# Kernel tuning notes

Measured on AMD Instinct MI355X. Metric: run time of the kernel, lower is better.

## Reference

```python
import jax, jax.numpy as jnp
import numpy as np

# Model constants (match init_kwargs)
IN_DIM = 1024   # input_dim == OLA frame size
ST_DIM = 128    # state_dim
HOP = IN_DIM // 2
N_FRAMES = 512
N_SAMPLES = 262144  # n_frames * hop
CTX = 512       # context_dim == control_plane_dim
HD = 32         # hypernetwork_dim
HL = 16         # hypernetwork_latent
B = 8


def _make_w(hv, A, Bm, i, o):
    # HyperNetworkLayer: hypervector -> latent -> flattened (i, o) matrix per batch
    return (hv @ A @ Bm).reshape(-1, i, o)


def setup_inputs() -> dict:
    key = jax.random.key(0)
    ks = jax.random.split(key, 17)
    s = 0.05
    return {
        'control_signal': jax.random.normal(ks[0], (B, CTX, N_FRAMES), jnp.float32),
        'state_hv': jax.random.normal(ks[1], (B, HD), jnp.float32),
        'output_hv': jax.random.normal(ks[2], (B, HD), jnp.float32),
        'input_hv': jax.random.normal(ks[3], (B, HD), jnp.float32),
        'direct_hv': jax.random.normal(ks[4], (B, HD), jnp.float32),
        'proj_hv': jax.random.normal(ks[5], (B, HD), jnp.float32),
        'times': jax.random.normal(ks[6], (B, 1, N_FRAMES), jnp.float32),
        # hypernetwork parameters (learned)
        'A_proj': jax.random.normal(ks[7], (HD, HL), jnp.float32) * s,
        'B_proj': jax.random.normal(ks[8], (HL, CTX * IN_DIM), jnp.float32) * s,
        'A_state': jax.random.normal(ks[9], (HD, HL), jnp.float32) * s,
        'B_state': jax.random.normal(ks[10], (HL, ST_DIM * ST_DIM), jnp.float32) * s,
        'A_input': jax.random.normal(ks[11], (HD, HL), jnp.float32) * s,
        'B_input': jax.random.normal(ks[12], (HL, IN_DIM * ST_DIM), jnp.float32) * s,
        'A_output': jax.random.normal(ks[13], (HD, HL), jnp.float32) * s,
        'B_output': jax.random.normal(ks[14], (HL, ST_DIM * IN_DIM), jnp.float32) * s,
        'A_direct': jax.random.normal(ks[15], (HD, HL), jnp.float32) * s,
        'B_direct': jax.random.normal(ks[16], (HL, IN_DIM * IN_DIM), jnp.float32) * s,
    }


def _forward(control_signal, state_hv, output_hv, input_hv, direct_hv, proj_hv, times,
             A_proj, B_proj, A_state, B_state, A_input, B_input,
             A_output, B_output, A_direct, B_direct):
    batch = control_signal.shape[0]
    dt = control_signal.dtype
    # per-batch hypernetwork-generated dense matrices
    Wp = _make_w(proj_hv, A_proj, B_proj, CTX, IN_DIM)       # [b, ctx, in]
    Ws = _make_w(state_hv, A_state, B_state, ST_DIM, ST_DIM)  # [b, st, st]
    Wi = _make_w(input_hv, A_input, B_input, IN_DIM, ST_DIM)  # [b, in, st]
    Wo = _make_w(output_hv, A_output, B_output, ST_DIM, IN_DIM)
    Wd = _make_w(direct_hv, A_direct, B_direct, IN_DIM, IN_DIM)

    ctrl = jnp.transpose(control_signal ** 2, (0, 2, 1))       # [b, fr, ctx]
    proj = jnp.einsum('bfc,bci->bfi', ctrl, Wp)                # [b, fr, in]

    def step(s, u):
        # s_i = A s_{i-1} + B u_i ; y_i = C (A s_{i-1}) + D u_i
        s2 = jnp.einsum('bs,bst->bt', s, Ws)
        y = jnp.einsum('bt,bti->bi', s2, Wo) + jnp.einsum('bi,bij->bj', u, Wd)
        s_new = s2 + jnp.einsum('bi,bis->bs', u, Wi)
        return s_new, y

    s0 = jnp.zeros((batch, ST_DIM), dt)
    _, outs = jax.lax.scan(step, s0, jnp.transpose(proj, (1, 0, 2)))  # [fr, b, in]
    outs = jnp.transpose(outs, (1, 0, 2))                              # [b, fr, in]

    # overlap-add with periodic hann window, hop = in_dim // 2
    win = 0.5 - 0.5 * jnp.cos(2.0 * jnp.pi * jnp.arange(IN_DIM, dtype=dt) / IN_DIM)
    windowed = outs * win
    total = HOP * (N_FRAMES - 1) + IN_DIM
    idx = jnp.arange(N_FRAMES)[:, None] * HOP + jnp.arange(IN_DIM)[None, :]  # [fr, in]
    buf = jnp.zeros((batch, total), dt).at[:, idx].add(windowed)
    sig = buf[:, :N_SAMPLES][:, None, :]   # [b, 1, n_samples]

    # DiracScheduler.schedule: softmax impulses over frames, upsample, FFT convolve
    impulses = jax.nn.softmax(times, axis=-1)                  # [b, 1, fr]
    up = jnp.zeros((batch, 1, N_SAMPLES), dt).at[:, :, ::N_SAMPLES // N_FRAMES].set(impulses)
    n = 2 * N_SAMPLES
    y = jnp.fft.irfft(jnp.fft.rfft(sig, n=n) * jnp.fft.rfft(up, n=n), n=n)[..., :N_SAMPLES]
    return y.astype(dt)


def reference(control_signal, state_hv, output_hv, input_hv, direct_hv, proj_hv, times,
              A_proj, B_proj, A_state, B_state, A_input, B_input,
              A_output, B_output, A_direct, B_direct):
    return _forward(control_signal, state_hv, output_hv, input_hv, direct_hv, proj_hv, times,
                    A_proj, B_proj, A_state, B_state, A_input, B_input,
                    A_output, B_output, A_direct, B_direct)
```

## Files before the change

kernel.cpp:

```cpp
#include <hip/hip_runtime.h>
#include <math.h>


typedef __attribute__((ext_vector_type(8))) short bfrag;
typedef __attribute__((ext_vector_type(4))) float f32x4;

__device__ inline unsigned short f2bf(float f) {
  unsigned int u = __float_as_uint(f);
  unsigned int r = (u + 0x7fff + ((u >> 16) & 1)) >> 16;
  return (unsigned short)r;
}

static const size_t OFF_LAT   = 0;
static const size_t OFF_IMP   = 1024;
static const size_t OFF_WSM   = 8192;
static const size_t OFF_WPT   = 139264;
static const size_t OFF_WOT   = 2236416;
static const size_t OFF_WDIT  = 2760704;
static const size_t OFF_CTRLT = 7479296;
static const size_t OFF_PROJ  = 8527872;
static const size_t OFF_PROJD = 10625024;
static const size_t OFF_S2    = 15343616;
static const size_t OFF_MPOW  = 15605760;
static const size_t OFF_EC    = 16785408;
static const size_t OFF_HC    = 16850944;
static const size_t OFF_Y     = 16916480;
static const size_t OFF_SIG   = 21110784;
static const size_t OFF_T     = 23207936;

__global__ void latents_kernel(
    const float* __restrict__ hv_p, const float* __restrict__ hv_s,
    const float* __restrict__ hv_i, const float* __restrict__ hv_o,
    const float* __restrict__ hv_d,
    const float* __restrict__ A_p, const float* __restrict__ A_s,
    const float* __restrict__ A_i, const float* __restrict__ A_o,
    const float* __restrict__ A_d,
    float* __restrict__ lat) {
  int tid = threadIdx.x;
  if (tid >= 640) return;
  int m = tid >> 7, b = (tid >> 4) & 7, l = tid & 15;
  const float* hv; const float* A;
  switch (m) {
    case 0: hv = hv_p; A = A_p; break;
    case 1: hv = hv_s; A = A_s; break;
    case 2: hv = hv_i; A = A_i; break;
    case 3: hv = hv_o; A = A_o; break;
    default: hv = hv_d; A = A_d; break;
  }
  float acc = 0.f;
  for (int h = 0; h < 32; ++h) acc = fmaf(hv[b * 32 + h], A[h * 16 + l], acc);
  lat[tid] = acc;
}

__global__ __launch_bounds__(256) void build_w_kernel(
    const float* __restrict__ lat,
    const float* __restrict__ Bm,
    float* __restrict__ out,
    int total, size_t bstride) {
  int e = (blockIdx.x * 256 + threadIdx.x) * 4;
  if (e >= total) return;
  float4 v[16];
#pragma unroll
  for (int l = 0; l < 16; ++l)
    v[l] = *(const float4*)(Bm + (size_t)l * total + e);
#pragma unroll 1
  for (int b = 0; b < 8; ++b) {
    float ax = 0.f, ay = 0.f, az = 0.f, aw = 0.f;
#pragma unroll
    for (int l = 0; l < 16; ++l) {
      float lv = lat[b * 16 + l];
      ax = fmaf(lv, v[l].x, ax);
      ay = fmaf(lv, v[l].y, ay);
      az = fmaf(lv, v[l].z, az);
      aw = fmaf(lv, v[l].w, aw);
    }
    *(float4*)(out + (size_t)b * bstride + e) = make_float4(ax, ay, az, aw);
  }
}

__global__ __launch_bounds__(256) void build_wt_kernel(
    const float* __restrict__ lat,
    const float* __restrict__ Bm,
    unsigned short* __restrict__ out,
    int R, int C, size_t bstride) {
  __shared__ float ls[128];
  __shared__ unsigned short tile[32][36];
  int tid = threadIdx.x;
  if (tid < 128) ls[tid] = lat[tid];
  int cc = tid & 31, rg = tid >> 5;
  int c = blockIdx.x * 32 + cc;
  int r0 = blockIdx.y * 32 + rg * 4;
  size_t RC = (size_t)R * C;
  float bm[16][4];
#pragma unroll
  for (int l = 0; l < 16; ++l) {
    const float* p = Bm + (size_t)l * RC + (size_t)r0 * C + c;
#pragma unroll
    for (int j = 0; j < 4; ++j) bm[l][j] = p[(size_t)j * C];
  }
  int wc = tid >> 3, wrq = tid & 7;
  __syncthreads();
#pragma unroll 1
  for (int b = 0; b < 8; ++b) {
    float a0 = 0.f, a1 = 0.f, a2 = 0.f, a3 = 0.f;
#pragma unroll
    for (int l = 0; l < 16; ++l) {
      float lv = ls[b * 16 + l];
      a0 = fmaf(lv, bm[l][0], a0);
      a1 = fmaf(lv, bm[l][1], a1);
      a2 = fmaf(lv, bm[l][2], a2);
      a3 = fmaf(lv, bm[l][3], a3);
    }
    __syncthreads();
    ushort2 p0, p1;
    p0.x = f2bf(a0); p0.y = f2bf(a1);
    p1.x = f2bf(a2); p1.y = f2bf(a3);
    *(ushort2*)&tile[cc][rg * 4] = p0;
    *(ushort2*)&tile[cc][rg * 4 + 2] = p1;
    __syncthreads();
    ushort4 v = *(const ushort4*)&tile[wc][wrq * 4];
    *(ushort4*)(out + (size_t)b * bstride +
                (size_t)(blockIdx.x * 32 + wc) * R + blockIdx.y * 32 + wrq * 4) = v;
  }
}

__global__ void transpose_sq_kernel(const float* __restrict__ in,
                                    unsigned short* __restrict__ out) {
  __shared__ float tile[32][33];
  int b = blockIdx.z;
  int c0 = blockIdx.x * 32, f0 = blockIdx.y * 32;
  int tx = threadIdx.x, ty = threadIdx.y;
  const float* inb = in + (size_t)b * 512 * 512;
  unsigned short* outb = out + (size_t)b * 512 * 512;
#pragma unroll
  for (int i = 0; i < 4; ++i) {
    float v = inb[(size_t)(c0 + ty + i * 8) * 512 + f0 + tx];
    tile[ty + i * 8][tx] = v * v;
  }
  __syncthreads();
#pragma unroll
  for (int i = 0; i < 4; ++i)
    outb[(size_t)(f0 + ty + i * 8) * 512 + c0 + tx] = f2bf(tile[tx][ty + i * 8]);
}

template <int EPI, int CD_BF16, int TRI>
__global__ __launch_bounds__(256) void mfma_gemm_kernel(
    const unsigned short* __restrict__ A,
    const unsigned short* __restrict__ BT,
    const float* __restrict__ D, int ldd,
    void* __restrict__ Cout,
    int M, int N, int K) {
  const int b = blockIdx.z;
  A  += (size_t)b * M * K;
  BT += (size_t)b * N * K;
  const int m0 = blockIdx.y * 128;
  const int n0 = blockIdx.x * 128;
  __shared__ __align__(16) unsigned short As[128][40];
  __shared__ __align__(16) unsigned short Bs[128][40];
  const int tid = threadIdx.x;
  const int lane = tid & 63, wave = tid >> 6;
  const int wr = (wave >> 1) * 64, wc = (wave & 1) * 64;
  const int l15 = lane & 15, g = lane >> 4;
  f32x4 acc[4][4];
#pragma unroll
  for (int i = 0; i < 4; ++i)
#pragma unroll
    for (int j = 0; j < 4; ++j)
#pragma unroll
      for (int r = 0; r < 4; ++r) acc[i][j][r] = 0.f;

  const int srow = tid >> 2, soct = tid & 3;
  const unsigned short* Ag = A + (size_t)(m0 + srow) * K + soct * 8;
  const unsigned short* Bg = BT + (size_t)(n0 + srow) * K + soct * 8;
  const size_t row64 = (size_t)64 * K;
  const int kend = TRI ? (m0 + 128) : K;

  for (int k0 = 0; k0 < kend; k0 += 32) {
    bfrag av0 = *(const bfrag*)(Ag + k0);
    bfrag av1 = *(const bfrag*)(Ag + row64 + k0);
    bfrag bv0 = *(const bfrag*)(Bg + k0);
    bfrag bv1 = *(const bfrag*)(Bg + row64 + k0);
    __syncthreads();
    *(bfrag*)(&As[srow][soct * 8]) = av0;
    *(bfrag*)(&As[64 + srow][soct * 8]) = av1;
    *(bfrag*)(&Bs[srow][soct * 8]) = bv0;
    *(bfrag*)(&Bs[64 + srow][soct * 8]) = bv1;
    __syncthreads();
    bfrag af[4], bf[4];
#pragma unroll
    for (int mi = 0; mi < 4; ++mi)
      af[mi] = *(const bfrag*)(&As[wr + mi * 16 + l15][g * 8]);
#pragma unroll
    for (int nj = 0; nj < 4; ++nj)
      bf[nj] = *(const bfrag*)(&Bs[wc + nj * 16 + l15][g * 8]);
#pragma unroll
    for (int mi = 0; mi < 4; ++mi)
#pragma unroll
      for (int nj = 0; nj < 4; ++nj)
        acc[mi][nj] = __builtin_amdgcn_mfma_f32_16x16x32_bf16(af[mi], bf[nj], acc[mi][nj], 0, 0, 0);
  }

  float* Cf = (float*)Cout + (size_t)b * M * N;
  unsigned short* Cb = (unsigned short*)Cout + (size_t)b * M * N;
  if (EPI) D += (size_t)b * M * ldd;
#pragma unroll
  for (int nj = 0; nj < 4; ++nj) {
    int n = n0 + wc + nj * 16 + l15;
    float win = 0.f;
    if (EPI) win = 0.5f - 0.5f * cosf(6.28318530717958647693f * (float)n / 1024.0f);
#pragma unroll
    for (int mi = 0; mi < 4; ++mi) {
      int mbase = m0 + wr + mi * 16 + 4 * g;
#pragma unroll
      for (int r = 0; r < 4; ++r) {
        int m = mbase + r;
        float v = acc[mi][nj][r];
        if (EPI) v = (v + D[(size_t)m * ldd + n]) * win;
        if (CD_BF16) Cb[(size_t)m * N + n] = f2bf(v);
        else         Cf[(size_t)m * N + n] = v;
      }
    }
  }
}

__global__ void copym1_kernel(const float* __restrict__ Wsm, float* __restrict__ Mpow) {
  int i = blockIdx.x * 256 + threadIdx.x;
  int b = i >> 12, r = i & 4095;
  *(float4*)(Mpow + ((size_t)b * 9 + 1) * 16384 + (size_t)r * 4) =
      *(const float4*)(Wsm + (size_t)b * 16384 + (size_t)r * 4);
}

__global__ __launch_bounds__(256) void powers_kernel(float* __restrict__ Mpow, int half) {
  int z = blockIdx.x;
  int b = z / half, k = z - b * half + 1;
  const float* A = Mpow + ((size_t)b * 9 + k) * 16384;
  const float* Bm = Mpow + ((size_t)b * 9 + half) * 16384;
  float* C = Mpow + ((size_t)b * 9 + half + k) * 16384;
  __shared__ __align__(16) float As[16][132];
  __shared__ __align__(16) float Bs[16][132];
  int tid = threadIdx.x;
  int tx = tid & 15, ty = tid >> 4;
  float acc[8][8];
#pragma unroll
  for (int i = 0; i < 8; ++i)
#pragma unroll
    for (int j = 0; j < 8; ++j) acc[i][j] = 0.f;
  int ar = tid >> 1, ac = (tid & 1) * 8;
  int br = tid >> 4, bc = (tid & 15) * 8;
  for (int k0 = 0; k0 < 128; k0 += 16) {
    float4 a0 = *(const float4*)(A + (size_t)ar * 128 + k0 + ac);
    float4 a1 = *(const float4*)(A + (size_t)ar * 128 + k0 + ac + 4);
    float4 b0 = *(const float4*)(Bm + (size_t)(k0 + br) * 128 + bc);
    float4 b1 = *(const float4*)(Bm + (size_t)(k0 + br) * 128 + bc + 4);
    __syncthreads();
    As[ac + 0][ar] = a0.x; As[ac + 1][ar] = a0.y; As[ac + 2][ar] = a0.z; As[ac + 3][ar] = a0.w;
    As[ac + 4][ar] = a1.x; As[ac + 5][ar] = a1.y; As[ac + 6][ar] = a1.z; As[ac + 7][ar] = a1.w;
    *(float4*)(&Bs[br][bc]) = b0;
    *(float4*)(&Bs[br][bc + 4]) = b1;
    __syncthreads();
#pragma unroll
    for (int kk = 0; kk < 16; ++kk) {
      float4 av0 = *(const float4*)(&As[kk][ty * 8]);
      float4 av1 = *(const float4*)(&As[kk][ty * 8 + 4]);
      float4 bv0 = *(const float4*)(&Bs[kk][tx * 8]);
      float4 bv1 = *(const float4*)(&Bs[kk][tx * 8 + 4]);
      float aa[8] = {av0.x, av0.y, av0.z, av0.w, av1.x, av1.y, av1.z, av1.w};
      float bb[8] = {bv0.x, bv0.y, bv0.z, bv0.w, bv1.x, bv1.y, bv1.z, bv1.w};
#pragma unroll
      for (int i = 0; i < 8; ++i)
#pragma unroll
        for (int j = 0; j < 8; ++j) acc[i][j] = fmaf(aa[i], bb[j], acc[i][j]);
    }
  }
#pragma unroll
  for (int i = 0; i < 8; ++i) {
    *(float4*)(C + (size_t)(ty * 8 + i) * 128 + tx * 8) =
        make_float4(acc[i][0], acc[i][1], acc[i][2], acc[i][3]);
    *(float4*)(C + (size_t)(ty * 8 + i) * 128 + tx * 8 + 4) =
        make_float4(acc[i][4], acc[i][5], acc[i][6], acc[i][7]);
  }
}

__global__ __launch_bounds__(256) void ec_kernel(
    const float* __restrict__ Mpow, const float* __restrict__ PD,
    float* __restrict__ Ec) {
  int b = blockIdx.x >> 6, c = blockIdx.x & 63;
  int tid = threadIdx.x, t = tid & 127, dh = tid >> 7;
  __shared__ __align__(16) float Bus[7][128];
  __shared__ float red[128];
  const float* Bu = PD + (size_t)b * 512 * 1152 + 1024;
  for (int idx = tid; idx < 896; idx += 256)
    Bus[idx >> 7][idx & 127] = Bu[(size_t)(c * 8 + (idx >> 7)) * 1152 + (idx & 127)];
  __syncthreads();
  float acc = 0.f;
  const float* Mb = Mpow + (size_t)b * 9 * 16384;
  int d0 = dh * 64;
#pragma unroll
  for (int i = 0; i < 7; ++i) {
    const float* Mk = Mb + (size_t)(7 - i) * 16384 + t;
#pragma unroll 8
    for (int d = 0; d < 64; ++d)
      acc = fmaf(Bus[i][d0 + d], Mk[(size_t)(d0 + d) * 128], acc);
  }
  if (dh == 1) red[t] = acc;
  __syncthreads();
  if (dh == 0) {
    float tot = acc + red[t] + Bu[(size_t)(c * 8 + 7) * 1152 + t];
    Ec[((size_t)b * 64 + c) * 128 + t] = tot;
  }
}

__global__ __launch_bounds__(128) void combine_kernel(
    const float* __restrict__ Mpow, const float* __restrict__ Ec,
    float* __restrict__ Hc) {
  int b = blockIdx.x, t = threadIdx.x;
  float w[128];
  const float* M8 = Mpow + ((size_t)b * 9 + 8) * 16384;
#pragma unroll
  for (int k = 0; k < 128; ++k) w[k] = M8[(size_t)k * 128 + t];
  __shared__ __align__(16) float sh[128];
  sh[t] = 0.f;
  Hc[((size_t)b * 64) * 128 + t] = 0.f;
  __syncthreads();
#pragma unroll 1
  for (int c = 0; c < 63; ++c) {
    float a0 = 0.f, a1 = 0.f, a2 = 0.f, a3 = 0.f;
#pragma unroll
    for (int k = 0; k < 128; k += 4) {
      float4 sv = *(const float4*)(&sh[k]);
      a0 = fmaf(sv.x, w[k + 0], a0);
      a1 = fmaf(sv.y, w[k + 1], a1);
      a2 = fmaf(sv.z, w[k + 2], a2);
      a3 = fmaf(sv.w, w[k + 3], a3);
    }
    float hn = (a0 + a1) + (a2 + a3) + Ec[((size_t)b * 64 + c) * 128 + t];
    __syncthreads();
    sh[t] = hn;
    __syncthreads();
    Hc[((size_t)b * 64 + c + 1) * 128 + t] = hn;
  }
}

__global__ __launch_bounds__(256) void pass2_kernel(
    const float* __restrict__ Mpow, const float* __restrict__ PD,
    const float* __restrict__ Hc, unsigned short* __restrict__ S2) {
  int b = blockIdx.x >> 6, c = blockIdx.x & 63;
  int tid = threadIdx.x, t = tid & 127, dh = tid >> 7;
  __shared__ __align__(16) float Xs[15][128];
  __shared__ __align__(16) float red[8][128];
  const float* Bu = PD + (size_t)b * 512 * 1152 + 1024;
  for (int idx = tid; idx < 15 * 128; idx += 256) {
    int rr = idx >> 7, cc = idx & 127;
    float v = 0.f;
    if (rr == 7) v = Hc[((size_t)b * 64 + c) * 128 + cc];
    else if (rr > 7) v = Bu[(size_t)(c * 8 + rr - 8) * 1152 + cc];
    Xs[rr][cc] = v;
  }
  __syncthreads();
  float acc[8];
#pragma unroll
  for (int j = 0; j < 8; ++j) acc[j] = 0.f;
  const float* Mb = Mpow + (size_t)b * 9 * 16384;
  int d0 = dh * 64;
#pragma unroll 1
  for (int k = 1; k <= 8; ++k) {
    const float* Mk = Mb + (size_t)k * 16384 + t;
    const int xbase = 8 - k;
#pragma unroll 4
    for (int d4 = 0; d4 < 16; ++d4) {
      int d = d0 + d4 * 4;
      float m0 = Mk[(size_t)(d + 0) * 128];
      float m1 = Mk[(size_t)(d + 1) * 128];
      float m2 = Mk[(size_t)(d + 2) * 128];
      float m3 = Mk[(size_t)(d + 3) * 128];
#pragma unroll
      for (int j = 0; j < 8; ++j) {
        float4 xv = *(const float4*)(&Xs[xbase + j][d]);
        acc[j] = fmaf(xv.x, m0, acc[j]);
        acc[j] = fmaf(xv.y, m1, acc[j]);
        acc[j] = fmaf(xv.z, m2, acc[j]);
        acc[j] = fmaf(xv.w, m3, acc[j]);
      }
    }
  }
  if (dh == 1) {
#pragma unroll
    for (int j = 0; j < 8; ++j) red[j][t] = acc[j];
  }
  __syncthreads();
  if (dh == 0) {
    unsigned short* S2b = S2 + ((size_t)b * 512 + c * 8) * 128;
#pragma unroll
    for (int j = 0; j < 8; ++j)
      S2b[(size_t)j * 128 + t] = f2bf(acc[j] + red[j][t]);
  }
}

__global__ void softmax_kernel(const float* __restrict__ times, float* __restrict__ imp) {
  int b = blockIdx.x, t = threadIdx.x;
  __shared__ float red[512];
  float v = times[b * 512 + t];
  red[t] = v;
  __syncthreads();
  for (int s = 256; s > 0; s >>= 1) {
    if (t < s) red[t] = fmaxf(red[t], red[t + s]);
    __syncthreads();
  }
  float m = red[0];
  __syncthreads();
  float e = expf(v - m);
  red[t] = e;
  __syncthreads();
  for (int s = 256; s > 0; s >>= 1) {
    if (t < s) red[t] += red[t + s];
    __syncthreads();
  }
  imp[b * 512 + t] = e / red[0];
}

__global__ void toeplitz_kernel(const float* __restrict__ imp, unsigned short* __restrict__ T) {
  int idx = blockIdx.x * 256 + threadIdx.x;
  int b = idx >> 16;
  int rem = idx & 65535;
  int q = rem >> 7, p4 = (rem & 127) * 4;
  const float* impb = imp + b * 512;
  ushort4 o;
  o.x = (p4 + 0 <= q) ? f2bf(impb[q - p4 - 0]) : (unsigned short)0;
  o.y = (p4 + 1 <= q) ? f2bf(impb[q - p4 - 1]) : (unsigned short)0;
  o.z = (p4 + 2 <= q) ? f2bf(impb[q - p4 - 2]) : (unsigned short)0;
  o.w = (p4 + 3 <= q) ? f2bf(impb[q - p4 - 3]) : (unsigned short)0;
  *(ushort4*)(T + ((size_t)b * 512 + q) * 512 + p4) = o;
}

__global__ __launch_bounds__(256) void ola_t_kernel(const float* __restrict__ Y,
                                                    unsigned short* __restrict__ sigT) {
  __shared__ unsigned short tile[64][72];
  int b = blockIdx.z;
  int q0 = blockIdx.x * 64, r0 = blockIdx.y * 64;
  int tid = threadIdx.x;
  int rr = tid & 63, qg = tid >> 6;
  const float* Yb = Y + (size_t)b * 512 * 1024;
#pragma unroll
  for (int i = 0; i < 16; ++i) {
    int q = q0 + qg * 16 + i;
    float v = Yb[(size_t)q * 1024 + r0 + rr];
    if (q > 0) v += Yb[(size_t)(q - 1) * 1024 + 512 + r0 + rr];
    tile[qg * 16 + i][rr] = f2bf(v);
  }
  __syncthreads();
  int rw = tid >> 2, qo = tid & 3;
  unsigned short* outb = sigT + ((size_t)b * 512 + r0 + rw) * 512 + q0;
  *(bfrag*)(outb + qo * 16) = *(const bfrag*)&tile[qo * 16][0] ;
}


extern "C" void kernel_launch(void* const* d_in, const int* in_sizes, int n_in,
                              void* d_out, int out_size, void* d_ws, size_t ws_size,
                              hipStream_t stream);

__global__ __launch_bounds__(256) void ola_transpose_kernel(const float* __restrict__ Y,
                                                            unsigned short* __restrict__ sigT) {
  __shared__ unsigned short tile[64][72];
  int b = blockIdx.z;
  int q0 = blockIdx.x * 64, r0 = blockIdx.y * 64;
  int tid = threadIdx.x;
  int rr = tid & 63, qg = tid >> 6;
  const float* Yb = Y + (size_t)b * 512 * 1024;
#pragma unroll
  for (int i = 0; i < 16; ++i) {
    int q = q0 + qg * 16 + i;
    float v = Yb[(size_t)q * 1024 + r0 + rr];
    if (q > 0) v += Yb[(size_t)(q - 1) * 1024 + 512 + r0 + rr];
    tile[qg * 16 + i][rr] = f2bf(v);
  }
  __syncthreads();
  int rw = tid >> 2, qo = tid & 3;
  unsigned short* orow = sigT + ((size_t)b * 512 + r0 + rw) * 512 + q0 + qo * 16;
  ushort4 w0, w1, w2, w3;
  w0.x = tile[qo * 16 + 0][rw];  w0.y = tile[qo * 16 + 1][rw];
  w0.z = tile[qo * 16 + 2][rw];  w0.w = tile[qo * 16 + 3][rw];
  w1.x = tile[qo * 16 + 4][rw];  w1.y = tile[qo * 16 + 5][rw];
  w1.z = tile[qo * 16 + 6][rw];  w1.w = tile[qo * 16 + 7][rw];
  w2.x = tile[qo * 16 + 8][rw];  w2.y = tile[qo * 16 + 9][rw];
  w2.z = tile[qo * 16 + 10][rw]; w2.w = tile[qo * 16 + 11][rw];
  w3.x = tile[qo * 16 + 12][rw]; w3.y = tile[qo * 16 + 13][rw];
  w3.z = tile[qo * 16 + 14][rw]; w3.w = tile[qo * 16 + 15][rw];
  *(ushort4*)(orow + 0)  = w0;
  *(ushort4*)(orow + 4)  = w1;
  *(ushort4*)(orow + 8)  = w2;
  *(ushort4*)(orow + 12) = w3;
}

extern "C" void kernel_launch(void* const* d_in, const int* in_sizes, int n_in,
                              void* d_out, int out_size, void* d_ws, size_t ws_size,
                              hipStream_t stream) {
  const float* control   = (const float*)d_in[0];
  const float* state_hv  = (const float*)d_in[1];
  const float* output_hv = (const float*)d_in[2];
  const float* input_hv  = (const float*)d_in[3];
  const float* direct_hv = (const float*)d_in[4];
  const float* proj_hv   = (const float*)d_in[5];
  const float* times     = (const float*)d_in[6];
  const float* A_proj   = (const float*)d_in[7];
  const float* B_proj   = (const float*)d_in[8];
  const float* A_state  = (const float*)d_in[9];
  const float* B_state  = (const float*)d_in[10];
  const float* A_input  = (const float*)d_in[11];
  const float* B_input  = (const float*)d_in[12];
  const float* A_output = (const float*)d_in[13];
  const float* B_output = (const float*)d_in[14];
  const float* A_direct = (const float*)d_in[15];
  const float* B_direct = (const float*)d_in[16];

  float* ws = (float*)d_ws;
  float* lat  = ws + OFF_LAT;
  float* impw = ws + OFF_IMP;
  float* Wsm  = ws + OFF_WSM;
  unsigned short* WpT   = (unsigned short*)(ws + OFF_WPT);
  unsigned short* WoT   = (unsigned short*)(ws + OFF_WOT);
  unsigned short* WdiT  = (unsigned short*)(ws + OFF_WDIT);
  unsigned short* ctrlT = (unsigned short*)(ws + OFF_CTRLT);
  unsigned short* proj  = (unsigned short*)(ws + OFF_PROJ);
  float* projD = ws + OFF_PROJD;
  unsigned short* S2 = (unsigned short*)(ws + OFF_S2);
  float* Mpow = ws + OFF_MPOW;
  float* Ec   = ws + OFF_EC;
  float* Hc   = ws + OFF_HC;
  float* Y    = ws + OFF_Y;
  unsigned short* sigT = (unsigned short*)(ws + OFF_SIG);
  unsigned short* Tb   = (unsigned short*)(ws + OFF_T);
  float* out  = (float*)d_out;

  latents_kernel<<<1, 640, 0, stream>>>(proj_hv, state_hv, input_hv, output_hv, direct_hv,
                                        A_proj, A_state, A_input, A_output, A_direct, lat);

  build_w_kernel<<<16, 256, 0, stream>>>(lat + 1 * 128, B_state, Wsm, 16384, 16384);

  build_wt_kernel<<<dim3(32, 16), 256, 0, stream>>>(lat + 0 * 128, B_proj, WpT, 512, 1024, 524288);
  build_wt_kernel<<<dim3(32, 32), 256, 0, stream>>>(lat + 4 * 128, B_direct, WdiT, 1024, 1024, 1179648);
  build_wt_kernel<<<dim3(4, 32), 256, 0, stream>>>(lat + 2 * 128, B_input, WdiT + 1024 * 1024, 1024, 128, 1179648);
  build_wt_kernel<<<dim3(32, 4), 256, 0, stream>>>(lat + 3 * 128, B_output, WoT, 128, 1024, 131072);

  transpose_sq_kernel<<<dim3(16, 16, 8), dim3(32, 8), 0, stream>>>(control, ctrlT);

  mfma_gemm_kernel<0, 1, 0><<<dim3(8, 4, 8), 256, 0, stream>>>(
      ctrlT, WpT, nullptr, 0, proj, 512, 1024, 512);

  mfma_gemm_kernel<0, 0, 0><<<dim3(9, 4, 8), 256, 0, stream>>>(
      proj, WdiT, nullptr, 0, projD, 512, 1152, 1024);

  copym1_kernel<<<128, 256, 0, stream>>>(Wsm, Mpow);
  powers_kernel<<<8, 256, 0, stream>>>(Mpow, 1);
  powers_kernel<<<16, 256, 0, stream>>>(Mpow, 2);
  powers_kernel<<<32, 256, 0, stream>>>(Mpow, 4);
  ec_kernel<<<512, 256, 0, stream>>>(Mpow, projD, Ec);
  combine_kernel<<<8, 128, 0, stream>>>(Mpow, Ec, Hc);
  pass2_kernel<<<512, 256, 0, stream>>>(Mpow, projD, Hc, S2);

  mfma_gemm_kernel<1, 0, 0><<<dim3(8, 4, 8), 256, 0, stream>>>(
      S2, WoT, projD, 1152, Y, 512, 1024, 128);

  softmax_kernel<<<8, 512, 0, stream>>>(times, impw);
  toeplitz_kernel<<<2048, 256, 0, stream>>>(impw, Tb);

  ola_transpose_kernel<<<dim3(8, 8, 8), 256, 0, stream>>>(Y, sigT);

  mfma_gemm_kernel<0, 0, 1><<<dim3(4, 4, 8), 256, 0, stream>>>(
      Tb, sigT, nullptr, 0, out, 512, 512, 512);
}
```

Measured before the change: 291.3 us.

## Double-buffer GEMM LDS tiles, streamline combine recurrence, and write state matrix directly into powers

The bf16 MFMA GEMM now uses two LDS buffers and prefetches the next K-tile into registers while the current tile is computed, cutting one barrier per iteration. The serial combine recurrence preloads its whole Ec slice into shared memory and ping-pongs the hidden state between two shared buffers, so each step needs one barrier instead of two. build_w writes the state matrix straight into slot 1 of Mpow with a per-batch stride, which removes the copy kernel and its launch. Double buffering doubles GEMM LDS use, and the combine kernel now takes 32KB of shared memory, which could lower occupancy.

```diff
diff --git a/kernel.cpp b/kernel.cpp
--- a/kernel.cpp
+++ b/kernel.cpp
@@ -13,7 +13,6 @@
 
 static const size_t OFF_LAT   = 0;
 static const size_t OFF_IMP   = 1024;
-static const size_t OFF_WSM   = 8192;
 static const size_t OFF_WPT   = 139264;
 static const size_t OFF_WOT   = 2236416;
 static const size_t OFF_WDIT  = 2760704;
@@ -155,8 +154,8 @@
   BT += (size_t)b * N * K;
   const int m0 = blockIdx.y * 128;
   const int n0 = blockIdx.x * 128;
-  __shared__ __align__(16) unsigned short As[128][40];
-  __shared__ __align__(16) unsigned short Bs[128][40];
+  __shared__ __align__(16) unsigned short As[2][128][40];
+  __shared__ __align__(16) unsigned short Bs[2][128][40];
   const int tid = threadIdx.x;
   const int lane = tid & 63, wave = tid >> 6;
   const int wr = (wave >> 1) * 64, wc = (wave & 1) * 64;
@@ -174,30 +173,41 @@
   const unsigned short* Bg = BT + (size_t)(n0 + srow) * K + soct * 8;
   const size_t row64 = (size_t)64 * K;
   const int kend = TRI ? (m0 + 128) : K;
-
-  for (int k0 = 0; k0 < kend; k0 += 32) {
-    bfrag av0 = *(const bfrag*)(Ag + k0);
-    bfrag av1 = *(const bfrag*)(Ag + row64 + k0);
-    bfrag bv0 = *(const bfrag*)(Bg + k0);
-    bfrag bv1 = *(const bfrag*)(Bg + row64 + k0);
-    __syncthreads();
-    *(bfrag*)(&As[srow][soct * 8]) = av0;
-    *(bfrag*)(&As[64 + srow][soct * 8]) = av1;
-    *(bfrag*)(&Bs[srow][soct * 8]) = bv0;
-    *(bfrag*)(&Bs[64 + srow][soct * 8]) = bv1;
-    __syncthreads();
+  const int nt = kend >> 5;
+
+  bfrag av0 = *(const bfrag*)(Ag);
+  bfrag av1 = *(const bfrag*)(Ag + row64);
+  bfrag bv0 = *(const bfrag*)(Bg);
+  bfrag bv1 = *(const bfrag*)(Bg + row64);
+
+  int cur = 0;
+#pragma unroll 1
+  for (int t = 0; t < nt; ++t) {
+    *(bfrag*)(&As[cur][srow][soct * 8]) = av0;
+    *(bfrag*)(&As[cur][64 + srow][soct * 8]) = av1;
+    *(bfrag*)(&Bs[cur][srow][soct * 8]) = bv0;
+    *(bfrag*)(&Bs[cur][64 + srow][soct * 8]) = bv1;
+    __syncthreads();
+    if (t + 1 < nt) {
+      const int k0 = (t + 1) << 5;
+      av0 = *(const bfrag*)(Ag + k0);
+      av1 = *(const bfrag*)(Ag + row64 + k0);
+      bv0 = *(const bfrag*)(Bg + k0);
+      bv1 = *(const bfrag*)(Bg + row64 + k0);
+    }
     bfrag af[4], bf[4];
 #pragma unroll
     for (int mi = 0; mi < 4; ++mi)
-      af[mi] = *(const bfrag*)(&As[wr + mi * 16 + l15][g * 8]);
+      af[mi] = *(const bfrag*)(&As[cur][wr + mi * 16 + l15][g * 8]);
 #pragma unroll
     for (int nj = 0; nj < 4; ++nj)
-      bf[nj] = *(const bfrag*)(&Bs[wc + nj * 16 + l15][g * 8]);
+      bf[nj] = *(const bfrag*)(&Bs[cur][wc + nj * 16 + l15][g * 8]);
 #pragma unroll
     for (int mi = 0; mi < 4; ++mi)
 #pragma unroll
       for (int nj = 0; nj < 4; ++nj)
         acc[mi][nj] = __builtin_amdgcn_mfma_f32_16x16x32_bf16(af[mi], bf[nj], acc[mi][nj], 0, 0, 0);
+    cur ^= 1;
   }
 
   float* Cf = (float*)Cout + (size_t)b * M * N;
@@ -221,13 +231,6 @@
       }
     }
   }
-}
-
-__global__ void copym1_kernel(const float* __restrict__ Wsm, float* __restrict__ Mpow) {
-  int i = blockIdx.x * 256 + threadIdx.x;
-  int b = i >> 12, r = i & 4095;
-  *(float4*)(Mpow + ((size_t)b * 9 + 1) * 16384 + (size_t)r * 4) =
-      *(const float4*)(Wsm + (size_t)b * 16384 + (size_t)r * 4);
 }
 
 __global__ __launch_bounds__(256) void powers_kernel(float* __restrict__ Mpow, int half) {
@@ -318,26 +321,35 @@
   const float* M8 = Mpow + ((size_t)b * 9 + 8) * 16384;
 #pragma unroll
   for (int k = 0; k < 128; ++k) w[k] = M8[(size_t)k * 128 + t];
-  __shared__ __align__(16) float sh[128];
-  sh[t] = 0.f;
-  Hc[((size_t)b * 64) * 128 + t] = 0.f;
-  __syncthreads();
+  __shared__ __align__(16) float ec_sh[64 * 128];
+  const float* Ecb = Ec + (size_t)b * 8192;
+#pragma unroll
+  for (int i = 0; i < 16; ++i) {
+    int idx = (t + i * 128) * 4;
+    *(float4*)&ec_sh[idx] = *(const float4*)(Ecb + idx);
+  }
+  __shared__ __align__(16) float sh[2][128];
+  sh[0][t] = 0.f;
+  float* Hcb = Hc + (size_t)b * 8192;
+  Hcb[t] = 0.f;
+  __syncthreads();
+  int cur = 0;
 #pragma unroll 1
   for (int c = 0; c < 63; ++c) {
     float a0 = 0.f, a1 = 0.f, a2 = 0.f, a3 = 0.f;
 #pragma unroll
     for (int k = 0; k < 128; k += 4) {
-      float4 sv = *(const float4*)(&sh[k]);
+      float4 sv = *(const float4*)(&sh[cur][k]);
       a0 = fmaf(sv.x, w[k + 0], a0);
       a1 = fmaf(sv.y, w[k + 1], a1);
       a2 = fmaf(sv.z, w[k + 2], a2);
       a3 = fmaf(sv.w, w[k + 3], a3);
     }
-    float hn = (a0 + a1) + (a2 + a3) + Ec[((size_t)b * 64 + c) * 128 + t];
-    __syncthreads();
-    sh[t] = hn;
-    __syncthreads();
-    Hc[((size_t)b * 64 + c + 1) * 128 + t] = hn;
+    float hn = (a0 + a1) + (a2 + a3) + ec_sh[c * 128 + t];
+    sh[cur ^ 1][t] = hn;
+    Hcb[(c + 1) * 128 + t] = hn;
+    __syncthreads();
+    cur ^= 1;
   }
 }
 
@@ -431,32 +443,6 @@
   o.w = (p4 + 3 <= q) ? f2bf(impb[q - p4 - 3]) : (unsigned short)0;
   *(ushort4*)(T + ((size_t)b * 512 + q) * 512 + p4) = o;
 }
-
-__global__ __launch_bounds__(256) void ola_t_kernel(const float* __restrict__ Y,
-                                                    unsigned short* __restrict__ sigT) {
-  __shared__ unsigned short tile[64][72];
-  int b = blockIdx.z;
-  int q0 = blockIdx.x * 64, r0 = blockIdx.y * 64;
-  int tid = threadIdx.x;
-  int rr = tid & 63, qg = tid >> 6;
-  const float* Yb = Y + (size_t)b * 512 * 1024;
-#pragma unroll
-  for (int i = 0; i < 16; ++i) {
-    int q = q0 + qg * 16 + i;
-    float v = Yb[(size_t)q * 1024 + r0 + rr];
-    if (q > 0) v += Yb[(size_t)(q - 1) * 1024 + 512 + r0 + rr];
-    tile[qg * 16 + i][rr] = f2bf(v);
-  }
-  __syncthreads();
-  int rw = tid >> 2, qo = tid & 3;
-  unsigned short* outb = sigT + ((size_t)b * 512 + r0 + rw) * 512 + q0;
-  *(bfrag*)(outb + qo * 16) = *(const bfrag*)&tile[qo * 16][0] ;
-}
-
-
-extern "C" void kernel_launch(void* const* d_in, const int* in_sizes, int n_in,
-                              void* d_out, int out_size, void* d_ws, size_t ws_size,
-                              hipStream_t stream);
 
 __global__ __launch_bounds__(256) void ola_transpose_kernel(const float* __restrict__ Y,
                                                             unsigned short* __restrict__ sigT) {
@@ -515,7 +501,6 @@
   float* ws = (float*)d_ws;
   float* lat  = ws + OFF_LAT;
   float* impw = ws + OFF_IMP;
-  float* Wsm  = ws + OFF_WSM;
   unsigned short* WpT   = (unsigned short*)(ws + OFF_WPT);
   unsigned short* WoT   = (unsigned short*)(ws + OFF_WOT);
   unsigned short* WdiT  = (unsigned short*)(ws + OFF_WDIT);
@@ -534,7 +519,7 @@
   latents_kernel<<<1, 640, 0, stream>>>(proj_hv, state_hv, input_hv, output_hv, direct_hv,
                                         A_proj, A_state, A_input, A_output, A_direct, lat);
 
-  build_w_kernel<<<16, 256, 0, stream>>>(lat + 1 * 128, B_state, Wsm, 16384, 16384);
+  build_w_kernel<<<16, 256, 0, stream>>>(lat + 1 * 128, B_state, Mpow + 16384, 16384, 147456);
 
   build_wt_kernel<<<dim3(32, 16), 256, 0, stream>>>(lat + 0 * 128, B_proj, WpT, 512, 1024, 524288);
   build_wt_kernel<<<dim3(32, 32), 256, 0, stream>>>(lat + 4 * 128, B_direct, WdiT, 1024, 1024, 1179648);
@@ -549,7 +534,6 @@
   mfma_gemm_kernel<0, 0, 0><<<dim3(9, 4, 8), 256, 0, stream>>>(
       proj, WdiT, nullptr, 0, projD, 512, 1152, 1024);
 
-  copym1_kernel<<<128, 256, 0, stream>>>(Wsm, Mpow);
   powers_kernel<<<8, 256, 0, stream>>>(Mpow, 1);
   powers_kernel<<<16, 256, 0, stream>>>(Mpow, 2);
   powers_kernel<<<32, 256, 0, stream>>>(Mpow, 4);
```

After: 272.4 us. -6.5%, faster.
